# Optimization experiments

Measured on AMD Instinct MI355X. Metric: run time of the kernel, lower is better.

The kernel has to match this reference:

```python
import jax, jax.numpy as jnp
import numpy as np


def _up(x, h, w):
    # bicubic (Keys a=-0.5, matching PIL BICUBIC) resize of [B,H,W] -> [B,h,w]
    return jax.image.resize(x, (x.shape[0], h, w), method='cubic')


def setup_inputs() -> dict:
    key = jax.random.key(0)
    ks = jax.random.split(key, 10)
    B = 64
    inp = {
        'cam_256': jax.random.uniform(ks[0], (B, 256, 256), dtype=jnp.float32),
        'cam_128': jax.random.uniform(ks[1], (B, 128, 128), dtype=jnp.float32),
        'cam_64':  jax.random.uniform(ks[2], (B, 64, 64), dtype=jnp.float32),
        'cam_32':  jax.random.uniform(ks[3], (B, 32, 32), dtype=jnp.float32),
        'w1': jax.random.normal(ks[4], (2,), dtype=jnp.float32),
        'b1': jax.random.normal(ks[5], (1,), dtype=jnp.float32),
        'w2': jax.random.normal(ks[6], (2,), dtype=jnp.float32),
        'b2': jax.random.normal(ks[7], (1,), dtype=jnp.float32),
        'w3': jax.random.normal(ks[8], (2,), dtype=jnp.float32),
        'b3': jax.random.normal(ks[9], (1,), dtype=jnp.float32),
    }
    return inp


def reference(cam_256, cam_128, cam_64, cam_32, w1, b1, w2, b2, w3, b3):
    B = cam_32.shape[0]
    # stage 1: up(32->64), concat with cam_64, 1x1 conv(2->1) + ReLU
    up32 = _up(cam_32, 64, 64)                              # [B,64,64]
    h64 = jax.nn.relu(w1[0] * up32 + w1[1] * cam_64 + b1[0])
    # stage 2: up(64->128), concat with cam_128, 1x1 conv + ReLU
    up64 = _up(h64, 128, 128)
    h128 = jax.nn.relu(w2[0] * up64 + w2[1] * cam_128 + b2[0])
    # stage 3: up(128->256), concat with cam_256, 1x1 conv + ReLU
    up128 = _up(h128, 256, 256)
    h256 = jax.nn.relu(w3[0] * up128 + w3[1] * cam_256 + b3[0])
    # final: bicubic up to 1024; original loop prepends each new image,
    # reversing batch order -> replicate with flip
    out = _up(h256, 1024, 1024)                             # [B,1024,1024]
    out = jnp.flip(out, axis=0)[:, None]                    # [B,1,1024,1024]
    return out
```

## Files before the change

### kernel.cpp

```cpp
#include <hip/hip_runtime.h>

typedef float vfloat4 __attribute__((ext_vector_type(4)));

__device__ __forceinline__ void taps4(int i, int n, float inv, int idx[4], float w[4]) {
  float s = ((float)i + 0.5f) * inv - 0.5f;
  int k0 = (int)floorf(s);
  float sum = 0.f;
#pragma unroll
  for (int t = 0; t < 4; ++t) {
    int j = k0 - 1 + t;
    float d = fabsf(s - (float)j);
    float wt = (d <= 1.f) ? (((1.5f * d - 2.5f) * d) * d + 1.f)
                          : (((-0.5f * d + 2.5f) * d - 4.f) * d + 2.f);
    if (j < 0 || j >= n) wt = 0.f;
    idx[t] = (j < 0) ? 0 : ((j >= n) ? n - 1 : j);
    w[t] = wt;
    sum += wt;
  }
  float r = 1.f / sum;
#pragma unroll
  for (int t = 0; t < 4; ++t) w[t] *= r;
}

#define W0_0 (-0.0439453125f)
#define W0_1 ( 0.3896484375f)
#define W0_2 ( 0.7275390625f)
#define W0_3 (-0.0732421875f)
#define W1_0 (-0.0068359375f)
#define W1_1 ( 0.0908203125f)
#define W1_2 ( 0.9638671875f)
#define W1_3 (-0.0478515625f)

#define U_0 (-0.0234375f)
#define U_1 ( 0.2265625f)
#define U_2 ( 0.8671875f)
#define U_3 (-0.0703125f)

__global__ void __launch_bounds__(256) up2_fuse_v2(const float* __restrict__ in, int n,
                                                   const float* __restrict__ cam,
                                                   const float* __restrict__ wv,
                                                   const float* __restrict__ bv,
                                                   float* __restrict__ out) {
  int g = blockIdx.x * 64 + threadIdx.x;
  int k = blockIdx.y * 4 + threadIdx.y;
  if (g >= n || k >= n) return;
  int b = blockIdx.z;
  const int no = 2 * n;
  const float* img = in + (size_t)b * n * n;

  float f[5][5];
#pragma unroll
  for (int i = 0; i < 5; ++i) {
    int r = k - 2 + i; r = r < 0 ? 0 : (r > n - 1 ? n - 1 : r);
    const float* rp = img + (size_t)r * n;
#pragma unroll
    for (int c = 0; c < 5; ++c) {
      int cc = g - 2 + c; cc = cc < 0 ? 0 : (cc > n - 1 ? n - 1 : cc);
      f[i][c] = rp[cc];
    }
  }

  float o[2][2];
  if (g >= 2 && g <= n - 3 && k >= 2 && k <= n - 3) {
    float v0[5], v1[5];
#pragma unroll
    for (int c = 0; c < 5; ++c) {
      v0[c] = U_0 * f[0][c] + U_1 * f[1][c] + U_2 * f[2][c] + U_3 * f[3][c];
      v1[c] = U_3 * f[1][c] + U_2 * f[2][c] + U_1 * f[3][c] + U_0 * f[4][c];
    }
    o[0][0] = U_0 * v0[0] + U_1 * v0[1] + U_2 * v0[2] + U_3 * v0[3];
    o[0][1] = U_3 * v0[1] + U_2 * v0[2] + U_1 * v0[3] + U_0 * v0[4];
    o[1][0] = U_0 * v1[0] + U_1 * v1[1] + U_2 * v1[2] + U_3 * v1[3];
    o[1][1] = U_3 * v1[1] + U_2 * v1[2] + U_1 * v1[3] + U_0 * v1[4];
  } else {
#pragma unroll
    for (int p = 0; p < 2; ++p) {
      int iyy[4]; float wy[4];
      taps4(2 * k + p, n, 0.5f, iyy, wy);
      float vv[5];
#pragma unroll
      for (int c = 0; c < 5; ++c)
        vv[c] = wy[0] * f[p][c] + wy[1] * f[p + 1][c] + wy[2] * f[p + 2][c] + wy[3] * f[p + 3][c];
#pragma unroll
      for (int q = 0; q < 2; ++q) {
        int ixx[4]; float wx[4];
        taps4(2 * g + q, n, 0.5f, ixx, wx);
        o[p][q] = wx[0] * vv[q] + wx[1] * vv[q + 1] + wx[2] * vv[q + 2] + wx[3] * vv[q + 3];
      }
    }
  }

  float c0 = wv[0], c1 = wv[1], cb = bv[0];
#pragma unroll
  for (int p = 0; p < 2; ++p) {
    size_t base = ((size_t)b * no + (2 * k + p)) * no + 2 * g;
    const float2 cm = *(const float2*)(cam + base);
    float2 r;
    r.x = fmaxf(c0 * o[p][0] + c1 * cm.x + cb, 0.f);
    r.y = fmaxf(c0 * o[p][1] + c1 * cm.y + cb, 0.f);
    *(float2*)(out + base) = r;
  }
}

__global__ void __launch_bounds__(256) up4_final_v2(const float* __restrict__ in,
                                                    float* __restrict__ out) {
  const int N = 256, NO = 1024, B = 64;
  int g = blockIdx.x * 64 + threadIdx.x;
  int k = blockIdx.y * 4 + threadIdx.y;
  int b = blockIdx.z;
  const float* img = in + (size_t)(B - 1 - b) * N * N;

  float f[5][5];
#pragma unroll
  for (int i = 0; i < 5; ++i) {
    int r = k - 2 + i; r = r < 0 ? 0 : (r > N - 1 ? N - 1 : r);
    const float* rp = img + (size_t)r * N;
#pragma unroll
    for (int c = 0; c < 5; ++c) {
      int cc = g - 2 + c; cc = cc < 0 ? 0 : (cc > N - 1 ? N - 1 : cc);
      f[i][c] = rp[cc];
    }
  }

  float o[4][4];
  if (g >= 2 && g <= N - 3 && k >= 2 && k <= N - 3) {
    float vy[4][5];
#pragma unroll
    for (int c = 0; c < 5; ++c) {
      vy[0][c] = W0_0 * f[0][c] + W0_1 * f[1][c] + W0_2 * f[2][c] + W0_3 * f[3][c];
      vy[1][c] = W1_0 * f[0][c] + W1_1 * f[1][c] + W1_2 * f[2][c] + W1_3 * f[3][c];
      vy[2][c] = W1_3 * f[1][c] + W1_2 * f[2][c] + W1_1 * f[3][c] + W1_0 * f[4][c];
      vy[3][c] = W0_3 * f[1][c] + W0_2 * f[2][c] + W0_1 * f[3][c] + W0_0 * f[4][c];
    }
#pragma unroll
    for (int p = 0; p < 4; ++p) {
      o[p][0] = W0_0 * vy[p][0] + W0_1 * vy[p][1] + W0_2 * vy[p][2] + W0_3 * vy[p][3];
      o[p][1] = W1_0 * vy[p][0] + W1_1 * vy[p][1] + W1_2 * vy[p][2] + W1_3 * vy[p][3];
      o[p][2] = W1_3 * vy[p][1] + W1_2 * vy[p][2] + W1_1 * vy[p][3] + W1_0 * vy[p][4];
      o[p][3] = W0_3 * vy[p][1] + W0_2 * vy[p][2] + W0_1 * vy[p][3] + W0_0 * vy[p][4];
    }
  } else {
#pragma unroll
    for (int p = 0; p < 4; ++p) {
      int iyy[4]; float wy[4];
      taps4(4 * k + p, N, 0.25f, iyy, wy);
      int oy = (p < 2) ? 0 : 1;
      float vv[5];
#pragma unroll
      for (int c = 0; c < 5; ++c)
        vv[c] = wy[0] * f[oy][c] + wy[1] * f[oy + 1][c] + wy[2] * f[oy + 2][c] + wy[3] * f[oy + 3][c];
#pragma unroll
      for (int q = 0; q < 4; ++q) {
        int ixx[4]; float wx[4];
        taps4(4 * g + q, N, 0.25f, ixx, wx);
        int ox = (q < 2) ? 0 : 1;
        o[p][q] = wx[0] * vv[ox] + wx[1] * vv[ox + 1] + wx[2] * vv[ox + 2] + wx[3] * vv[ox + 3];
      }
    }
  }

#pragma unroll
  for (int p = 0; p < 4; ++p) {
    vfloat4 vec = { o[p][0], o[p][1], o[p][2], o[p][3] };
    __builtin_nontemporal_store(vec, (vfloat4*)(out + ((size_t)b * NO + 4 * k + p) * NO + 4 * g));
  }
}

extern "C" void kernel_launch(void* const* d_in, const int* in_sizes, int n_in_,
                              void* d_out, int out_size, void* d_ws, size_t ws_size,
                              hipStream_t stream) {
  const float* cam256 = (const float*)d_in[0];
  const float* cam128 = (const float*)d_in[1];
  const float* cam64  = (const float*)d_in[2];
  const float* cam32  = (const float*)d_in[3];
  const float* w1 = (const float*)d_in[4];
  const float* b1 = (const float*)d_in[5];
  const float* w2 = (const float*)d_in[6];
  const float* b2 = (const float*)d_in[7];
  const float* w3 = (const float*)d_in[8];
  const float* b3 = (const float*)d_in[9];
  float* out = (float*)d_out;

  const int B = 64;
  float* h64  = (float*)d_ws;
  float* h128 = h64 + (size_t)B * 64 * 64;
  float* h256 = h128 + (size_t)B * 128 * 128;

  dim3 blk(64, 4, 1);
  up2_fuse_v2<<<dim3(1, 8, B),  blk, 0, stream>>>(cam32, 32, cam64, w1, b1, h64);
  up2_fuse_v2<<<dim3(1, 16, B), blk, 0, stream>>>(h64, 64, cam128, w2, b2, h128);
  up2_fuse_v2<<<dim3(2, 32, B), blk, 0, stream>>>(h128, 128, cam256, w3, b3, h256);
  up4_final_v2<<<dim3(4, 64, B), blk, 0, stream>>>(h256, out);
}
```

Before: 349.4 us.

## Fuse all four upsample stages into one kernel with shared-memory slab intermediates

Replaces four separate launches with a single kernel. Each block handles one 32-row slab of one image and recomputes the needed halo rows of the 64, 128 and 256 intermediates into shared memory, with a barrier between stages. This removes the global round-trips for the intermediate maps and three kernel launches. In exchange, halo rows are recomputed redundantly across slabs, the grid shrinks to 512 blocks of 512 threads, and about 53 KB of LDS per block may limit occupancy during the write-bound final stage.

Measured after the change: 332.6 us. -4.8%, faster.

```diff
diff --git a/kernel.cpp b/kernel.cpp
--- a/kernel.cpp
+++ b/kernel.cpp
@@ -2,7 +2,11 @@
 
 typedef float vfloat4 __attribute__((ext_vector_type(4)));
 
-__device__ __forceinline__ void taps4(int i, int n, float inv, int idx[4], float w[4]) {
+__device__ __forceinline__ int iclamp(int v, int lo, int hi) {
+  return v < lo ? lo : (v > hi ? hi : v);
+}
+
+__device__ __forceinline__ void taps4w(int i, int n, float inv, float w[4]) {
   float s = ((float)i + 0.5f) * inv - 0.5f;
   int k0 = (int)floorf(s);
   float sum = 0.f;
@@ -13,7 +17,6 @@
     float wt = (d <= 1.f) ? (((1.5f * d - 2.5f) * d) * d + 1.f)
                           : (((-0.5f * d + 2.5f) * d - 4.f) * d + 2.f);
     if (j < 0 || j >= n) wt = 0.f;
-    idx[t] = (j < 0) ? 0 : ((j >= n) ? n - 1 : j);
     w[t] = wt;
     sum += wt;
   }
@@ -30,37 +33,13 @@
 #define W1_1 ( 0.0908203125f)
 #define W1_2 ( 0.9638671875f)
 #define W1_3 (-0.0478515625f)
-
 #define U_0 (-0.0234375f)
 #define U_1 ( 0.2265625f)
 #define U_2 ( 0.8671875f)
 #define U_3 (-0.0703125f)
 
-__global__ void __launch_bounds__(256) up2_fuse_v2(const float* __restrict__ in, int n,
-                                                   const float* __restrict__ cam,
-                                                   const float* __restrict__ wv,
-                                                   const float* __restrict__ bv,
-                                                   float* __restrict__ out) {
-  int g = blockIdx.x * 64 + threadIdx.x;
-  int k = blockIdx.y * 4 + threadIdx.y;
-  if (g >= n || k >= n) return;
-  int b = blockIdx.z;
-  const int no = 2 * n;
-  const float* img = in + (size_t)b * n * n;
-
-  float f[5][5];
-#pragma unroll
-  for (int i = 0; i < 5; ++i) {
-    int r = k - 2 + i; r = r < 0 ? 0 : (r > n - 1 ? n - 1 : r);
-    const float* rp = img + (size_t)r * n;
-#pragma unroll
-    for (int c = 0; c < 5; ++c) {
-      int cc = g - 2 + c; cc = cc < 0 ? 0 : (cc > n - 1 ? n - 1 : cc);
-      f[i][c] = rp[cc];
-    }
-  }
-
-  float o[2][2];
+__device__ __forceinline__ void up2_cell(const float (&f)[5][5], int k, int g, int n,
+                                         float (&o)[2][2]) {
   if (g >= 2 && g <= n - 3 && k >= 2 && k <= n - 3) {
     float v0[5], v1[5];
 #pragma unroll
@@ -75,55 +54,25 @@
   } else {
 #pragma unroll
     for (int p = 0; p < 2; ++p) {
-      int iyy[4]; float wy[4];
-      taps4(2 * k + p, n, 0.5f, iyy, wy);
+      float wy[4];
+      taps4w(2 * k + p, n, 0.5f, wy);
       float vv[5];
 #pragma unroll
       for (int c = 0; c < 5; ++c)
         vv[c] = wy[0] * f[p][c] + wy[1] * f[p + 1][c] + wy[2] * f[p + 2][c] + wy[3] * f[p + 3][c];
 #pragma unroll
       for (int q = 0; q < 2; ++q) {
-        int ixx[4]; float wx[4];
-        taps4(2 * g + q, n, 0.5f, ixx, wx);
+        float wx[4];
+        taps4w(2 * g + q, n, 0.5f, wx);
         o[p][q] = wx[0] * vv[q] + wx[1] * vv[q + 1] + wx[2] * vv[q + 2] + wx[3] * vv[q + 3];
       }
     }
   }
-
-  float c0 = wv[0], c1 = wv[1], cb = bv[0];
-#pragma unroll
-  for (int p = 0; p < 2; ++p) {
-    size_t base = ((size_t)b * no + (2 * k + p)) * no + 2 * g;
-    const float2 cm = *(const float2*)(cam + base);
-    float2 r;
-    r.x = fmaxf(c0 * o[p][0] + c1 * cm.x + cb, 0.f);
-    r.y = fmaxf(c0 * o[p][1] + c1 * cm.y + cb, 0.f);
-    *(float2*)(out + base) = r;
-  }
-}
-
-__global__ void __launch_bounds__(256) up4_final_v2(const float* __restrict__ in,
-                                                    float* __restrict__ out) {
-  const int N = 256, NO = 1024, B = 64;
-  int g = blockIdx.x * 64 + threadIdx.x;
-  int k = blockIdx.y * 4 + threadIdx.y;
-  int b = blockIdx.z;
-  const float* img = in + (size_t)(B - 1 - b) * N * N;
-
-  float f[5][5];
-#pragma unroll
-  for (int i = 0; i < 5; ++i) {
-    int r = k - 2 + i; r = r < 0 ? 0 : (r > N - 1 ? N - 1 : r);
-    const float* rp = img + (size_t)r * N;
-#pragma unroll
-    for (int c = 0; c < 5; ++c) {
-      int cc = g - 2 + c; cc = cc < 0 ? 0 : (cc > N - 1 ? N - 1 : cc);
-      f[i][c] = rp[cc];
-    }
-  }
-
-  float o[4][4];
-  if (g >= 2 && g <= N - 3 && k >= 2 && k <= N - 3) {
+}
+
+__device__ __forceinline__ void up4_cell(const float (&f)[5][5], int k, int g, int n,
+                                         float (&o)[4][4]) {
+  if (g >= 2 && g <= n - 3 && k >= 2 && k <= n - 3) {
     float vy[4][5];
 #pragma unroll
     for (int c = 0; c < 5; ++c) {
@@ -142,8 +91,8 @@
   } else {
 #pragma unroll
     for (int p = 0; p < 4; ++p) {
-      int iyy[4]; float wy[4];
-      taps4(4 * k + p, N, 0.25f, iyy, wy);
+      float wy[4];
+      taps4w(4 * k + p, n, 0.25f, wy);
       int oy = (p < 2) ? 0 : 1;
       float vv[5];
 #pragma unroll
@@ -151,18 +100,143 @@
         vv[c] = wy[0] * f[oy][c] + wy[1] * f[oy + 1][c] + wy[2] * f[oy + 2][c] + wy[3] * f[oy + 3][c];
 #pragma unroll
       for (int q = 0; q < 4; ++q) {
-        int ixx[4]; float wx[4];
-        taps4(4 * g + q, N, 0.25f, ixx, wx);
+        float wx[4];
+        taps4w(4 * g + q, n, 0.25f, wx);
         int ox = (q < 2) ? 0 : 1;
         o[p][q] = wx[0] * vv[ox] + wx[1] * vv[ox + 1] + wx[2] * vv[ox + 2] + wx[3] * vv[ox + 3];
       }
     }
   }
-
-#pragma unroll
-  for (int p = 0; p < 4; ++p) {
-    vfloat4 vec = { o[p][0], o[p][1], o[p][2], o[p][3] };
-    __builtin_nontemporal_store(vec, (vfloat4*)(out + ((size_t)b * NO + 4 * k + p) * NO + 4 * g));
+}
+
+__global__ void __launch_bounds__(512, 4) fused_all(
+    const float* __restrict__ cam256, const float* __restrict__ cam128,
+    const float* __restrict__ cam64, const float* __restrict__ cam32,
+    const float* __restrict__ w1, const float* __restrict__ b1,
+    const float* __restrict__ w2, const float* __restrict__ b2,
+    const float* __restrict__ w3, const float* __restrict__ b3,
+    float* __restrict__ out) {
+  __shared__ float s_h64[16 * 64];
+  __shared__ float s_h128[24 * 128];
+  __shared__ float s_h256[36 * 256];
+
+  const int tid = threadIdx.x;
+  const int slab = blockIdx.x;
+  const int b = blockIdx.y;
+  const int s = slab * 32;
+
+  const int r_lo = s - 2 < 0 ? 0 : s - 2, r_hi = s + 33 > 255 ? 255 : s + 33;
+  const int kr0 = r_lo >> 1, kr1 = r_hi >> 1;
+  const int h256_row0 = 2 * kr0;
+  const int j_lo = kr0 - 2 < 0 ? 0 : kr0 - 2, j_hi = kr1 + 2 > 127 ? 127 : kr1 + 2;
+  const int kj0 = j_lo >> 1, kj1 = j_hi >> 1;
+  const int h128_row0 = 2 * kj0;
+  const int m_lo = kj0 - 2 < 0 ? 0 : kj0 - 2, m_hi = kj1 + 2 > 63 ? 63 : kj1 + 2;
+  const int km0 = m_lo >> 1, km1 = m_hi >> 1;
+  const int h64_row0 = 2 * km0;
+
+  const float w1_0 = w1[0], w1_1 = w1[1], b1_0 = b1[0];
+  const float w2_0 = w2[0], w2_1 = w2[1], b2_0 = b2[0];
+  const float w3_0 = w3[0], w3_1 = w3[1], b3_0 = b3[0];
+
+  {
+    const float* c32 = cam32 + (size_t)b * 32 * 32;
+    const float* c64 = cam64 + (size_t)b * 64 * 64;
+    const int nk = km1 - km0 + 1;
+    for (int idx = tid; idx < nk * 32; idx += 512) {
+      int k = km0 + (idx >> 5), g = idx & 31;
+      float f[5][5];
+#pragma unroll
+      for (int i = 0; i < 5; ++i) {
+        int r = iclamp(k - 2 + i, 0, 31);
+#pragma unroll
+        for (int c = 0; c < 5; ++c) f[i][c] = c32[r * 32 + iclamp(g - 2 + c, 0, 31)];
+      }
+      float o[2][2];
+      up2_cell(f, k, g, 32, o);
+#pragma unroll
+      for (int p = 0; p < 2; ++p)
+#pragma unroll
+        for (int q = 0; q < 2; ++q) {
+          int row = 2 * k + p, col = 2 * g + q;
+          float h = w1_0 * o[p][q] + w1_1 * c64[row * 64 + col] + b1_0;
+          s_h64[(row - h64_row0) * 64 + col] = fmaxf(h, 0.f);
+        }
+    }
+  }
+  __syncthreads();
+
+  {
+    const float* c128 = cam128 + (size_t)b * 128 * 128;
+    const int nk = kj1 - kj0 + 1;
+    for (int idx = tid; idx < nk * 64; idx += 512) {
+      int k = kj0 + (idx >> 6), g = idx & 63;
+      float f[5][5];
+#pragma unroll
+      for (int i = 0; i < 5; ++i) {
+        int r = iclamp(k - 2 + i, 0, 63) - h64_row0;
+#pragma unroll
+        for (int c = 0; c < 5; ++c) f[i][c] = s_h64[r * 64 + iclamp(g - 2 + c, 0, 63)];
+      }
+      float o[2][2];
+      up2_cell(f, k, g, 64, o);
+#pragma unroll
+      for (int p = 0; p < 2; ++p)
+#pragma unroll
+        for (int q = 0; q < 2; ++q) {
+          int row = 2 * k + p, col = 2 * g + q;
+          float h = w2_0 * o[p][q] + w2_1 * c128[row * 128 + col] + b2_0;
+          s_h128[(row - h128_row0) * 128 + col] = fmaxf(h, 0.f);
+        }
+    }
+  }
+  __syncthreads();
+
+  {
+    const float* c256 = cam256 + (size_t)b * 256 * 256;
+    const int nk = kr1 - kr0 + 1;
+    for (int idx = tid; idx < nk * 128; idx += 512) {
+      int k = kr0 + (idx >> 7), g = idx & 127;
+      float f[5][5];
+#pragma unroll
+      for (int i = 0; i < 5; ++i) {
+        int r = iclamp(k - 2 + i, 0, 127) - h128_row0;
+#pragma unroll
+        for (int c = 0; c < 5; ++c) f[i][c] = s_h128[r * 128 + iclamp(g - 2 + c, 0, 127)];
+      }
+      float o[2][2];
+      up2_cell(f, k, g, 128, o);
+#pragma unroll
+      for (int p = 0; p < 2; ++p)
+#pragma unroll
+        for (int q = 0; q < 2; ++q) {
+          int row = 2 * k + p, col = 2 * g + q;
+          float h = w3_0 * o[p][q] + w3_1 * c256[row * 256 + col] + b3_0;
+          s_h256[(row - h256_row0) * 256 + col] = fmaxf(h, 0.f);
+        }
+    }
+  }
+  __syncthreads();
+
+  {
+    float* outimg = out + (size_t)(63 - b) * 1024 * 1024;
+    for (int idx = tid; idx < 32 * 256; idx += 512) {
+      int k = s + (idx >> 8), g = idx & 255;
+      float f[5][5];
+#pragma unroll
+      for (int i = 0; i < 5; ++i) {
+        int r = iclamp(k - 2 + i, 0, 255) - h256_row0;
+#pragma unroll
+        for (int c = 0; c < 5; ++c) f[i][c] = s_h256[r * 256 + iclamp(g - 2 + c, 0, 255)];
+      }
+      float o[4][4];
+      up4_cell(f, k, g, 256, o);
+#pragma unroll
+      for (int p = 0; p < 4; ++p) {
+        vfloat4 v = {o[p][0], o[p][1], o[p][2], o[p][3]};
+        __builtin_nontemporal_store(v, (vfloat4*)(outimg + (size_t)(4 * k + p) * 1024 + 4 * g));
+      }
+    }
   }
 }
 
@@ -181,14 +255,6 @@
   const float* b3 = (const float*)d_in[9];
   float* out = (float*)d_out;
 
-  const int B = 64;
-  float* h64  = (float*)d_ws;
-  float* h128 = h64 + (size_t)B * 64 * 64;
-  float* h256 = h128 + (size_t)B * 128 * 128;
-
-  dim3 blk(64, 4, 1);
-  up2_fuse_v2<<<dim3(1, 8, B),  blk, 0, stream>>>(cam32, 32, cam64, w1, b1, h64);
-  up2_fuse_v2<<<dim3(1, 16, B), blk, 0, stream>>>(h64, 64, cam128, w2, b2, h128);
-  up2_fuse_v2<<<dim3(2, 32, B), blk, 0, stream>>>(h128, 128, cam256, w3, b3, h256);
-  up4_final_v2<<<dim3(4, 64, B), blk, 0, stream>>>(h256, out);
-}
+  fused_all<<<dim3(8, 64), 512, 0, stream>>>(cam256, cam128, cam64, cam32,
+                                             w1, b1, w2, b2, w3, b3, out);
+}
```
